# Kernel tuning notes

Measured on AMD Instinct MI355X. Metric: run time of the kernel, lower is better.

The kernel has to match this reference:

```python
import jax, jax.numpy as jnp
import numpy as np

N = 50000      # nodes
E = 500000     # edges
IN = 128       # in_channels
HID = 64       # hidden_channels
OUT = 128      # out_channels
H = 4          # heads
NEG_SLOPE = 0.2


def _glorot(key, shape):
    fan_in, fan_out = shape[0], shape[-1]
    lim = np.sqrt(6.0 / (fan_in + fan_out))
    return jax.random.uniform(key, shape, jnp.float32, -lim, lim)


def setup_inputs() -> dict:
    key = jax.random.key(0)
    ks = jax.random.split(key, 12)
    return {
        "x": jax.random.normal(ks[0], (N, IN), jnp.float32),
        "edge_index": jax.random.randint(ks[1], (2, E), 0, N, jnp.int64),
        "edge_weight": jax.random.uniform(ks[2], (E,), jnp.float32),
        # layer 1: IN -> H*HID
        "W1": _glorot(ks[3], (IN, H * HID)),
        "b1": jnp.zeros((H * HID,), jnp.float32),
        "att1": _glorot(ks[4], (H, HID)),
        # layer 2: HID -> H*HID  (update() means over heads -> HID features)
        "W2": _glorot(ks[5], (HID, H * HID)),
        "b2": jnp.zeros((H * HID,), jnp.float32),
        "att2": _glorot(ks[6], (H, HID)),
        # layer 3: HID -> H*OUT
        "W3": _glorot(ks[7], (HID, H * OUT)),
        "b3": jnp.zeros((H * OUT,), jnp.float32),
        "att3": _glorot(ks[8], (H, OUT)),
    }


def _gat_layer(x, W, b, att, src, dst, edge_weight, out_dim):
    # lin + reshape to [N, H, D]
    h = (x @ W + b).reshape(-1, H, out_dim)
    xj = h[src]                                   # gather source feats [E,H,D]
    alpha = jnp.sum(xj * att[None], axis=-1)      # per-edge att score [E,H]
    alpha = jax.nn.leaky_relu(alpha, NEG_SLOPE)
    alpha = alpha * edge_weight[:, None]
    alpha = jax.nn.softmax(alpha, axis=1)         # softmax over HEADS (dim=1, as in source)
    msg = xj * alpha[:, :, None]                  # [E,H,D]
    aggr = jax.ops.segment_sum(msg, dst, num_segments=N)  # scatter-add [N,H,D]
    return aggr.mean(axis=1)                      # update(): mean over heads -> [N,D]


def reference(x, edge_index, edge_weight, W1, b1, att1, W2, b2, att2, W3, b3, att3):
    src, dst = edge_index[0], edge_index[1]
    h = _gat_layer(x, W1, b1, att1, src, dst, edge_weight, HID)
    h = jax.nn.relu(h)
    h = _gat_layer(h, W2, b2, att2, src, dst, edge_weight, HID)
    h = jax.nn.relu(h)
    return _gat_layer(h, W3, b3, att3, src, dst, edge_weight, OUT)
```

## Files before the change

### kernel.cpp

```cpp
#include <hip/hip_runtime.h>
#include <hip/hip_bf16.h>

#define NHEAD 4
#define NEG 0.2f

typedef __bf16 bf16x8 __attribute__((ext_vector_type(8)));
typedef __bf16 bf16x4 __attribute__((ext_vector_type(4)));
typedef float f32x4 __attribute__((ext_vector_type(4)));

__device__ __forceinline__ float blo(unsigned u) { return __uint_as_float(u << 16); }
__device__ __forceinline__ float bhi(unsigned u) { return __uint_as_float(u & 0xffff0000u); }
__device__ __forceinline__ unsigned short fbits(float f) {
    __bf16 h = (__bf16)f;
    return *(unsigned short*)&h;
}


__global__ __launch_bounds__(256) void hist_k(const int* __restrict__ dst,
                                              int* __restrict__ deg, int E) {
    int e = blockIdx.x * 256 + threadIdx.x;
    if (e < E) atomicAdd(&deg[dst[e]], 1);
}

__global__ __launch_bounds__(256) void partial_k(const int* __restrict__ deg,
                                                 int* __restrict__ bsum, int n) {
    int t = threadIdx.x;
    int base = blockIdx.x * 2048 + t * 8;
    int s = 0;
#pragma unroll
    for (int i = 0; i < 8; ++i) {
        int idx = base + i;
        if (idx < n) s += deg[idx];
    }
#pragma unroll
    for (int off = 32; off; off >>= 1) s += __shfl_down(s, off, 64);
    __shared__ int ws[4];
    if ((t & 63) == 0) ws[t >> 6] = s;
    __syncthreads();
    if (t == 0) bsum[blockIdx.x] = ws[0] + ws[1] + ws[2] + ws[3];
}

__global__ __launch_bounds__(256) void bscan_k(const int* __restrict__ bsum,
                                               int* __restrict__ boff, int nb) {
    __shared__ int sh[256];
    int t = threadIdx.x;
    int v = (t < nb) ? bsum[t] : 0;
    sh[t] = v;
    __syncthreads();
    for (int off = 1; off < 256; off <<= 1) {
        int u = (t >= off) ? sh[t - off] : 0;
        __syncthreads();
        sh[t] += u;
        __syncthreads();
    }
    if (t < nb) boff[t] = sh[t] - v;
}

__global__ __launch_bounds__(256) void rescan_k(const int* __restrict__ deg,
                                                const int* __restrict__ boff,
                                                int* __restrict__ rowptr,
                                                int* __restrict__ fill,
                                                int n, int total) {
    __shared__ int ts[256];
    int t = threadIdx.x;
    int base = blockIdx.x * 2048 + t * 8;
    int v[8];
    int s = 0;
#pragma unroll
    for (int i = 0; i < 8; ++i) {
        int idx = base + i;
        v[i] = (idx < n) ? deg[idx] : 0;
        s += v[i];
    }
    ts[t] = s;
    __syncthreads();
    for (int off = 1; off < 256; off <<= 1) {
        int u = (t >= off) ? ts[t - off] : 0;
        __syncthreads();
        ts[t] += u;
        __syncthreads();
    }
    int run = boff[blockIdx.x] + ts[t] - s;
#pragma unroll
    for (int i = 0; i < 8; ++i) {
        int idx = base + i;
        if (idx < n) {
            rowptr[idx] = run;
            fill[idx] = run;
            run += v[i];
        }
    }
    if (blockIdx.x == 0 && t == 0) rowptr[n] = total;
}

__global__ __launch_bounds__(256) void scatter_k(const int* __restrict__ src,
                                                 const int* __restrict__ dst,
                                                 const float* __restrict__ ew,
                                                 int* __restrict__ fill,
                                                 int* __restrict__ srcs,
                                                 float* __restrict__ wsrt, int E) {
    int e = blockIdx.x * 256 + threadIdx.x;
    if (e < E) {
        int d = dst[e];
        int p = atomicAdd(&fill[d], 1);
        srcs[p] = src[e];
        wsrt[p] = ew[e];
    }
}


__global__ __launch_bounds__(256) void prep_k(const float* __restrict__ W1, const float* __restrict__ att1, const float* __restrict__ b1,
                                              const float* __restrict__ W2, const float* __restrict__ att2, const float* __restrict__ b2,
                                              const float* __restrict__ W3, const float* __restrict__ att3, const float* __restrict__ b3,
                                              float* __restrict__ v1, float* __restrict__ v2, float* __restrict__ v3,
                                              float* __restrict__ c1, float* __restrict__ c2, float* __restrict__ c3) {
    int tid = blockIdx.x * 256 + threadIdx.x;
    if (tid < 512) {
        int h = tid >> 7, k = tid & 127;
        float p = 0.f;
        for (int d = 0; d < 64; ++d) p += W1[k * 256 + h * 64 + d] * att1[h * 64 + d];
        v1[h * 128 + k] = p;
    } else if (tid < 768) {
        int t = tid - 512, h = t >> 6, k = t & 63;
        float p = 0.f;
        for (int d = 0; d < 64; ++d) p += W2[k * 256 + h * 64 + d] * att2[h * 64 + d];
        v2[h * 64 + k] = p;
    } else if (tid < 1024) {
        int t = tid - 768, h = t >> 6, k = t & 63;
        float p = 0.f;
        for (int d = 0; d < 128; ++d) p += W3[k * 512 + h * 128 + d] * att3[h * 128 + d];
        v3[h * 64 + k] = p;
    } else if (tid < 1028) {
        int h = tid - 1024;
        float p = 0.f;
        for (int d = 0; d < 64; ++d) p += b1[h * 64 + d] * att1[h * 64 + d];
        c1[h] = p;
    } else if (tid < 1032) {
        int h = tid - 1028;
        float p = 0.f;
        for (int d = 0; d < 64; ++d) p += b2[h * 64 + d] * att2[h * 64 + d];
        c2[h] = p;
    } else if (tid < 1036) {
        int h = tid - 1032;
        float p = 0.f;
        for (int d = 0; d < 128; ++d) p += b3[h * 128 + d] * att3[h * 128 + d];
        c3[h] = p;
    }
}


__global__ __launch_bounds__(256) void wpack3_k(const float* __restrict__ W1,
                                                const float* __restrict__ W2,
                                                const float* __restrict__ W3,
                                                unsigned short* __restrict__ Ws1,
                                                unsigned short* __restrict__ Ws2,
                                                unsigned short* __restrict__ Ws3) {
    int tid = blockIdx.x * 256 + threadIdx.x;
    if (tid < 32768) {
        int d = tid >> 9, r = tid & 511, h = r >> 7, k = r & 127;
        Ws1[tid] = fbits(W1[k * 256 + h * 64 + d]);
    } else if (tid < 49152) {
        int t = tid - 32768;
        int d = t >> 8, r = t & 255, h = r >> 6, k = r & 63;
        Ws2[t] = fbits(W2[k * 256 + h * 64 + d]);
    } else if (tid < 81920) {
        int t = tid - 49152;
        int d = t >> 8, r = t & 255, h = r >> 6, k = r & 63;
        Ws3[t] = fbits(W3[k * 512 + h * 128 + d]);
    }
}


__global__ __launch_bounds__(256) void xpack_score_k(const float* __restrict__ x,
                                                     const float* __restrict__ v1,
                                                     const float* __restrict__ c1,
                                                     unsigned* __restrict__ xb,
                                                     float* __restrict__ s, int n) {
    int gt = blockIdx.x * 256 + threadIdx.x;
    int node = gt >> 6, lane = gt & 63;
    if (node >= n) return;
    float2 xv = ((const float2*)(x + (size_t)node * 128))[lane];
    xb[(size_t)node * 64 + lane] = (unsigned)fbits(xv.x) | ((unsigned)fbits(xv.y) << 16);
    int d0 = 2 * lane;
    float p0 = xv.x * v1[0 * 128 + d0] + xv.y * v1[0 * 128 + d0 + 1];
    float p1 = xv.x * v1[1 * 128 + d0] + xv.y * v1[1 * 128 + d0 + 1];
    float p2 = xv.x * v1[2 * 128 + d0] + xv.y * v1[2 * 128 + d0 + 1];
    float p3 = xv.x * v1[3 * 128 + d0] + xv.y * v1[3 * 128 + d0 + 1];
#pragma unroll
    for (int off = 32; off; off >>= 1) {
        p0 += __shfl_xor(p0, off, 64);
        p1 += __shfl_xor(p1, off, 64);
        p2 += __shfl_xor(p2, off, 64);
        p3 += __shfl_xor(p3, off, 64);
    }
    if (lane == 0)
        *(float4*)&s[(size_t)node * 4] = make_float4(p0 + c1[0], p1 + c1[1], p2 + c1[2], p3 + c1[3]);
}


__global__ __launch_bounds__(256) void alpha_k(const int* __restrict__ srcs,
                                               const float* __restrict__ wsrt,
                                               const float* __restrict__ s,
                                               float* __restrict__ alpha, int E) {
    int e = blockIdx.x * 256 + threadIdx.x;
    if (e >= E) return;
    int sn = srcs[e];
    float w = wsrt[e];
    float4 sv = *(const float4*)&s[(size_t)sn * NHEAD];
    float a0 = (sv.x > 0.f ? sv.x : NEG * sv.x) * w;
    float a1 = (sv.y > 0.f ? sv.y : NEG * sv.y) * w;
    float a2 = (sv.z > 0.f ? sv.z : NEG * sv.z) * w;
    float a3 = (sv.w > 0.f ? sv.w : NEG * sv.w) * w;
    float m = fmaxf(fmaxf(a0, a1), fmaxf(a2, a3));
    float e0 = __expf(a0 - m), e1 = __expf(a1 - m);
    float e2 = __expf(a2 - m), e3 = __expf(a3 - m);
    float inv = 0.25f / (e0 + e1 + e2 + e3);
    *(float4*)&alpha[(size_t)e * 4] = make_float4(e0 * inv, e1 * inv, e2 * inv, e3 * inv);
}


template <int K, int D, bool LAST>
__global__ __launch_bounds__(256) void fused_k(const int* __restrict__ rowptr,
                                               const int* __restrict__ srcs,
                                               const float* __restrict__ alpha,
                                               const unsigned* __restrict__ xb,
                                               const unsigned short* __restrict__ Ws,
                                               const float* __restrict__ bias,
                                               const float* __restrict__ vnext,
                                               const float* __restrict__ cnext,
                                               unsigned short* __restrict__ aout,
                                               float* __restrict__ fout,
                                               float* __restrict__ snext,
                                               int n) {
    constexpr int HK = 4 * K;
    constexpr int KS = HK / 32;
    constexpr int NC = D / 16;
    constexpr int CW = NC / 4;
    constexpr int ROWB = HK + 8;
    constexpr int DW = K / 32;

    __shared__ __bf16 gh[16 * ROWB];
    __shared__ __bf16 gl[16 * ROWB];
    __shared__ float4 A_lds[16];
    __shared__ float4 sc_lds[4][16];

    int t = threadIdx.x;
    int r0 = blockIdx.x * 16;
    int n4 = t >> 4, sl = t & 15;
    int node = r0 + n4;

    float acc[4][2 * DW];
#pragma unroll
    for (int h = 0; h < 4; ++h)
#pragma unroll
        for (int j = 0; j < 2 * DW; ++j) acc[h][j] = 0.f;
    float4 aA = make_float4(0.f, 0.f, 0.f, 0.f);

    auto accum = [&](float4 al, const unsigned* u) {
#pragma unroll
        for (int j = 0; j < DW; ++j) {
            float x0 = blo(u[j]), x1 = bhi(u[j]);
            acc[0][2 * j] += al.x * x0; acc[0][2 * j + 1] += al.x * x1;
            acc[1][2 * j] += al.y * x0; acc[1][2 * j + 1] += al.y * x1;
            acc[2][2 * j] += al.z * x0; acc[2][2 * j + 1] += al.z * x1;
            acc[3][2 * j] += al.w * x0; acc[3][2 * j + 1] += al.w * x1;
        }
        aA.x += al.x; aA.y += al.y; aA.z += al.z; aA.w += al.w;
    };

    if (node < n) {
        int beg = rowptr[node], end = rowptr[node + 1];
        int e = beg;
        for (; e + 1 < end; e += 2) {
            int snA = srcs[e], snB = srcs[e + 1];
            float4 alA = *(const float4*)&alpha[(size_t)e * 4];
            float4 alB = *(const float4*)&alpha[(size_t)(e + 1) * 4];
            unsigned uA[DW], uB[DW];
            if constexpr (DW == 4) {
                uint4 ta = ((const uint4*)xb)[(size_t)snA * 16 + sl];
                uint4 tb = ((const uint4*)xb)[(size_t)snB * 16 + sl];
                uA[0] = ta.x; uA[1] = ta.y; uA[2] = ta.z; uA[3] = ta.w;
                uB[0] = tb.x; uB[1] = tb.y; uB[2] = tb.z; uB[3] = tb.w;
            } else {
                uint2 ta = ((const uint2*)xb)[(size_t)snA * 16 + sl];
                uint2 tb = ((const uint2*)xb)[(size_t)snB * 16 + sl];
                uA[0] = ta.x; uA[1] = ta.y;
                uB[0] = tb.x; uB[1] = tb.y;
            }
            accum(alA, uA);
            accum(alB, uB);
        }
        if (e < end) {
            int sn = srcs[e];
            float4 al = *(const float4*)&alpha[(size_t)e * 4];
            unsigned u[DW];
            if constexpr (DW == 4) {
                uint4 ta = ((const uint4*)xb)[(size_t)sn * 16 + sl];
                u[0] = ta.x; u[1] = ta.y; u[2] = ta.z; u[3] = ta.w;
            } else {
                uint2 ta = ((const uint2*)xb)[(size_t)sn * 16 + sl];
                u[0] = ta.x; u[1] = ta.y;
            }
            accum(al, u);
        }
    }

    {
        size_t gbase = (size_t)n4 * ROWB;
#pragma unroll
        for (int h = 0; h < 4; ++h) {
            if constexpr (DW == 4) {
                bf16x8 vh, vl;
#pragma unroll
                for (int j = 0; j < 8; ++j) {
                    __bf16 hi = (__bf16)acc[h][j];
                    vh[j] = hi;
                    vl[j] = (__bf16)(acc[h][j] - (float)hi);
                }
                *(bf16x8*)&gh[gbase + h * K + sl * 8] = vh;
                *(bf16x8*)&gl[gbase + h * K + sl * 8] = vl;
            } else {
                bf16x4 vh, vl;
#pragma unroll
                for (int j = 0; j < 4; ++j) {
                    __bf16 hi = (__bf16)acc[h][j];
                    vh[j] = hi;
                    vl[j] = (__bf16)(acc[h][j] - (float)hi);
                }
                *(bf16x4*)&gh[gbase + h * K + sl * 4] = vh;
                *(bf16x4*)&gl[gbase + h * K + sl * 4] = vl;
            }
        }
        if (sl == 0) A_lds[n4] = aA;
    }
    __syncthreads();

    int wid = t >> 6, lane = t & 63;
    int lrow = lane & 15, gq = lane >> 4;

    f32x4 acc2[CW];
#pragma unroll
    for (int cw = 0; cw < CW; ++cw)
#pragma unroll
        for (int r = 0; r < 4; ++r) acc2[cw][r] = 0.f;

    const __bf16* wsp = (const __bf16*)Ws;
#pragma unroll
    for (int ks = 0; ks < KS; ++ks) {
        bf16x8 fh = *(const bf16x8*)&gh[(size_t)lrow * ROWB + ks * 32 + gq * 8];
        bf16x8 fl = *(const bf16x8*)&gl[(size_t)lrow * ROWB + ks * 32 + gq * 8];
#pragma unroll
        for (int cw = 0; cw < CW; ++cw) {
            int c = wid * CW + cw;
            bf16x8 bfr = *(const bf16x8*)(wsp + (size_t)(c * 16 + lrow) * HK + ks * 32 + gq * 8);
            acc2[cw] = __builtin_amdgcn_mfma_f32_16x16x32_bf16(fh, bfr, acc2[cw], 0, 0, 0);
            acc2[cw] = __builtin_amdgcn_mfma_f32_16x16x32_bf16(fl, bfr, acc2[cw], 0, 0, 0);
        }
    }

    float4 Ar[4];
#pragma unroll
    for (int r = 0; r < 4; ++r) Ar[r] = A_lds[gq * 4 + r];

    float sc[4][4];
#pragma unroll
    for (int h = 0; h < 4; ++h)
#pragma unroll
        for (int r = 0; r < 4; ++r) sc[h][r] = 0.f;

#pragma unroll
    for (int cw = 0; cw < CW; ++cw) {
        int col = (wid * CW + cw) * 16 + lrow;
        float bb0 = bias[0 * D + col], bb1 = bias[1 * D + col];
        float bb2 = bias[2 * D + col], bb3 = bias[3 * D + col];
        float vv0 = 0.f, vv1 = 0.f, vv2 = 0.f, vv3 = 0.f;
        if constexpr (!LAST) {
            vv0 = vnext[0 * D + col]; vv1 = vnext[1 * D + col];
            vv2 = vnext[2 * D + col]; vv3 = vnext[3 * D + col];
        }
#pragma unroll
        for (int r = 0; r < 4; ++r) {
            float val = acc2[cw][r] + Ar[r].x * bb0 + Ar[r].y * bb1 + Ar[r].z * bb2 + Ar[r].w * bb3;
            int row = r0 + gq * 4 + r;
            if constexpr (LAST) {
                if (row < n) fout[(size_t)row * D + col] = val;
            } else {
                val = fmaxf(val, 0.f);
                if (row < n) aout[(size_t)row * D + col] = fbits(val);
                sc[0][r] += val * vv0;
                sc[1][r] += val * vv1;
                sc[2][r] += val * vv2;
                sc[3][r] += val * vv3;
            }
        }
    }

    if constexpr (!LAST) {
#pragma unroll
        for (int m = 1; m < 16; m <<= 1) {
#pragma unroll
            for (int h = 0; h < 4; ++h)
#pragma unroll
                for (int r = 0; r < 4; ++r) sc[h][r] += __shfl_xor(sc[h][r], m, 64);
        }
        if (lrow < 4) {
            int r = lrow;
            sc_lds[wid][gq * 4 + r] = make_float4(sc[0][r], sc[1][r], sc[2][r], sc[3][r]);
        }
        __syncthreads();
        if (t < 16) {
            int row = r0 + t;
            if (row < n) {
                float4 s0 = sc_lds[0][t], s1 = sc_lds[1][t];
                float4 s2 = sc_lds[2][t], s3 = sc_lds[3][t];
                *(float4*)&snext[(size_t)row * 4] =
                    make_float4(s0.x + s1.x + s2.x + s3.x + cnext[0],
                                s0.y + s1.y + s2.y + s3.y + cnext[1],
                                s0.z + s1.z + s2.z + s3.z + cnext[2],
                                s0.w + s1.w + s2.w + s3.w + cnext[3]);
            }
        }
    }
}


extern "C" void kernel_launch(void* const* d_in, const int* in_sizes, int n_in,
                              void* d_out, int out_size, void* d_ws, size_t ws_size,
                              hipStream_t stream) {
    const float* x    = (const float*)d_in[0];
    const int*   ei   = (const int*)d_in[1];
    const float* ew   = (const float*)d_in[2];
    const float* W1   = (const float*)d_in[3];
    const float* b1   = (const float*)d_in[4];
    const float* att1 = (const float*)d_in[5];
    const float* W2   = (const float*)d_in[6];
    const float* b2   = (const float*)d_in[7];
    const float* att2 = (const float*)d_in[8];
    const float* W3   = (const float*)d_in[9];
    const float* b3   = (const float*)d_in[10];
    const float* att3 = (const float*)d_in[11];

    const int N = in_sizes[0] / 128;
    const int E = in_sizes[2];
    const int* src = ei;
    const int* dst = ei + E;

    char* wp = (char*)d_ws;
    auto alloc = [&](size_t bytes) -> void* {
        void* p = (void*)wp;
        wp += (bytes + 511) & ~(size_t)511;
        return p;
    };
    int*   deg    = (int*)alloc((size_t)N * 4);
    int*   rowptr = (int*)alloc((size_t)(N + 1) * 4);
    int*   fill   = (int*)alloc((size_t)N * 4);
    int*   bsum   = (int*)alloc(256 * 4);
    int*   boff   = (int*)alloc(256 * 4);
    int*   srcs   = (int*)alloc((size_t)E * 4);
    float* wsrt   = (float*)alloc((size_t)E * 4);
    unsigned* xb  = (unsigned*)alloc((size_t)N * 64 * 4);
    float* s      = (float*)alloc((size_t)N * 4 * 4);
    float* alpha  = (float*)alloc((size_t)E * 4 * 4);
    unsigned short* a1 = (unsigned short*)alloc((size_t)N * 64 * 2);
    unsigned short* a2 = (unsigned short*)alloc((size_t)N * 64 * 2);
    float* v1 = (float*)alloc(512 * 4);
    float* v2 = (float*)alloc(256 * 4);
    float* v3 = (float*)alloc(256 * 4);
    float* c1 = (float*)alloc(16);
    float* c2 = (float*)alloc(16);
    float* c3 = (float*)alloc(16);
    unsigned short* Ws1 = (unsigned short*)alloc(32768 * 2);
    unsigned short* Ws2 = (unsigned short*)alloc(16384 * 2);
    unsigned short* Ws3 = (unsigned short*)alloc(32768 * 2);

    wpack3_k<<<320, 256, 0, stream>>>(W1, W2, W3, Ws1, Ws2, Ws3);
    prep_k<<<5, 256, 0, stream>>>(W1, att1, b1, W2, att2, b2, W3, att3, b3,
                                  v1, v2, v3, c1, c2, c3);
    int gx = (N * 64 + 255) / 256;
    xpack_score_k<<<gx, 256, 0, stream>>>(x, v1, c1, xb, s, N);

    hipMemsetAsync(deg, 0, (size_t)N * 4, stream);
    int ge = (E + 255) / 256;
    int nb = (N + 2047) / 2048;
    hist_k<<<ge, 256, 0, stream>>>(dst, deg, E);
    partial_k<<<nb, 256, 0, stream>>>(deg, bsum, N);
    bscan_k<<<1, 256, 0, stream>>>(bsum, boff, nb);
    rescan_k<<<nb, 256, 0, stream>>>(deg, boff, rowptr, fill, N, E);
    scatter_k<<<ge, 256, 0, stream>>>(src, dst, ew, fill, srcs, wsrt, E);

    int gf = (N + 15) / 16;

    alpha_k<<<ge, 256, 0, stream>>>(srcs, wsrt, s, alpha, E);
    fused_k<128, 64, false><<<gf, 256, 0, stream>>>(rowptr, srcs, alpha, xb, Ws1, b1,
                                                    v2, c2, a1, nullptr, s, N);

    alpha_k<<<ge, 256, 0, stream>>>(srcs, wsrt, s, alpha, E);
    fused_k<64, 64, false><<<gf, 256, 0, stream>>>(rowptr, srcs, alpha, (const unsigned*)a1,
                                                   Ws2, b2, v3, c3, a2, nullptr, s, N);

    alpha_k<<<ge, 256, 0, stream>>>(srcs, wsrt, s, alpha, E);
    fused_k<64, 128, true><<<gf, 256, 0, stream>>>(rowptr, srcs, alpha, (const unsigned*)a2,
                                                   Ws3, b3, nullptr, nullptr, nullptr,
                                                   (float*)d_out, nullptr, N);
}
```

Baseline: 253.8 us.

## Fuse per-edge alpha computation into aggregation kernel and swizzle LDS layout

Removes the separate alpha_k kernel and computes the per-edge softmax-over-heads inside the fused aggregation loop from the source node's score and the edge weight. A second score buffer is used to ping-pong, so no kernel reads and writes the same score array. The edge loop is unrolled to 4 edges, the LDS staging drops row padding in favour of an XOR swizzle to avoid bank conflicts, and launch bounds request 4 blocks per CU. This saves three kernel launches and the E*16-byte alpha write and read per layer, at the cost of recomputing exp per edge for each of the 16 threads handling a node.

```diff
diff --git a/kernel.cpp b/kernel.cpp
--- a/kernel.cpp
+++ b/kernel.cpp
@@ -198,15 +198,8 @@
 }
 
 
-__global__ __launch_bounds__(256) void alpha_k(const int* __restrict__ srcs,
-                                               const float* __restrict__ wsrt,
-                                               const float* __restrict__ s,
-                                               float* __restrict__ alpha, int E) {
-    int e = blockIdx.x * 256 + threadIdx.x;
-    if (e >= E) return;
-    int sn = srcs[e];
-    float w = wsrt[e];
-    float4 sv = *(const float4*)&s[(size_t)sn * NHEAD];
+__device__ __forceinline__ float4 edge_alpha(const float* __restrict__ s, int sn, float w) {
+    float4 sv = *(const float4*)&s[(size_t)sn * 4];
     float a0 = (sv.x > 0.f ? sv.x : NEG * sv.x) * w;
     float a1 = (sv.y > 0.f ? sv.y : NEG * sv.y) * w;
     float a2 = (sv.z > 0.f ? sv.z : NEG * sv.z) * w;
@@ -215,32 +208,32 @@
     float e0 = __expf(a0 - m), e1 = __expf(a1 - m);
     float e2 = __expf(a2 - m), e3 = __expf(a3 - m);
     float inv = 0.25f / (e0 + e1 + e2 + e3);
-    *(float4*)&alpha[(size_t)e * 4] = make_float4(e0 * inv, e1 * inv, e2 * inv, e3 * inv);
+    return make_float4(e0 * inv, e1 * inv, e2 * inv, e3 * inv);
 }
 
 
 template <int K, int D, bool LAST>
-__global__ __launch_bounds__(256) void fused_k(const int* __restrict__ rowptr,
-                                               const int* __restrict__ srcs,
-                                               const float* __restrict__ alpha,
-                                               const unsigned* __restrict__ xb,
-                                               const unsigned short* __restrict__ Ws,
-                                               const float* __restrict__ bias,
-                                               const float* __restrict__ vnext,
-                                               const float* __restrict__ cnext,
-                                               unsigned short* __restrict__ aout,
-                                               float* __restrict__ fout,
-                                               float* __restrict__ snext,
-                                               int n) {
+__global__ __launch_bounds__(256, 4) void fused_k(const int* __restrict__ rowptr,
+                                                  const int* __restrict__ srcs,
+                                                  const float* __restrict__ wsrt,
+                                                  const float* __restrict__ sprev,
+                                                  const unsigned* __restrict__ xb,
+                                                  const unsigned short* __restrict__ Ws,
+                                                  const float* __restrict__ bias,
+                                                  const float* __restrict__ vnext,
+                                                  const float* __restrict__ cnext,
+                                                  unsigned short* __restrict__ aout,
+                                                  float* __restrict__ fout,
+                                                  float* __restrict__ snext,
+                                                  int n) {
     constexpr int HK = 4 * K;
     constexpr int KS = HK / 32;
     constexpr int NC = D / 16;
     constexpr int CW = NC / 4;
-    constexpr int ROWB = HK + 8;
     constexpr int DW = K / 32;
 
-    __shared__ __bf16 gh[16 * ROWB];
-    __shared__ __bf16 gl[16 * ROWB];
+    __shared__ __bf16 gh[16 * HK];
+    __shared__ __bf16 gl[16 * HK];
     __shared__ float4 A_lds[16];
     __shared__ float4 sc_lds[4][16];
 
@@ -256,6 +249,15 @@
         for (int j = 0; j < 2 * DW; ++j) acc[h][j] = 0.f;
     float4 aA = make_float4(0.f, 0.f, 0.f, 0.f);
 
+    auto load_u = [&](int sn, unsigned* u) {
+        if constexpr (DW == 4) {
+            uint4 ta = ((const uint4*)xb)[(size_t)sn * 16 + sl];
+            u[0] = ta.x; u[1] = ta.y; u[2] = ta.z; u[3] = ta.w;
+        } else {
+            uint2 ta = ((const uint2*)xb)[(size_t)sn * 16 + sl];
+            u[0] = ta.x; u[1] = ta.y;
+        }
+    };
     auto accum = [&](float4 al, const unsigned* u) {
 #pragma unroll
         for (int j = 0; j < DW; ++j) {
@@ -271,42 +273,30 @@
     if (node < n) {
         int beg = rowptr[node], end = rowptr[node + 1];
         int e = beg;
-        for (; e + 1 < end; e += 2) {
-            int snA = srcs[e], snB = srcs[e + 1];
-            float4 alA = *(const float4*)&alpha[(size_t)e * 4];
-            float4 alB = *(const float4*)&alpha[(size_t)(e + 1) * 4];
-            unsigned uA[DW], uB[DW];
-            if constexpr (DW == 4) {
-                uint4 ta = ((const uint4*)xb)[(size_t)snA * 16 + sl];
-                uint4 tb = ((const uint4*)xb)[(size_t)snB * 16 + sl];
-                uA[0] = ta.x; uA[1] = ta.y; uA[2] = ta.z; uA[3] = ta.w;
-                uB[0] = tb.x; uB[1] = tb.y; uB[2] = tb.z; uB[3] = tb.w;
-            } else {
-                uint2 ta = ((const uint2*)xb)[(size_t)snA * 16 + sl];
-                uint2 tb = ((const uint2*)xb)[(size_t)snB * 16 + sl];
-                uA[0] = ta.x; uA[1] = ta.y;
-                uB[0] = tb.x; uB[1] = tb.y;
-            }
-            accum(alA, uA);
-            accum(alB, uB);
-        }
-        if (e < end) {
+        for (; e + 3 < end; e += 4) {
+            int sn0 = srcs[e], sn1 = srcs[e + 1], sn2 = srcs[e + 2], sn3 = srcs[e + 3];
+            float w0 = wsrt[e], w1 = wsrt[e + 1], w2 = wsrt[e + 2], w3 = wsrt[e + 3];
+            unsigned u0[DW], u1[DW], u2[DW], u3[DW];
+            load_u(sn0, u0); load_u(sn1, u1); load_u(sn2, u2); load_u(sn3, u3);
+            float4 al0 = edge_alpha(sprev, sn0, w0);
+            float4 al1 = edge_alpha(sprev, sn1, w1);
+            float4 al2 = edge_alpha(sprev, sn2, w2);
+            float4 al3 = edge_alpha(sprev, sn3, w3);
+            accum(al0, u0); accum(al1, u1); accum(al2, u2); accum(al3, u3);
+        }
+        for (; e < end; ++e) {
             int sn = srcs[e];
-            float4 al = *(const float4*)&alpha[(size_t)e * 4];
             unsigned u[DW];
-            if constexpr (DW == 4) {
-                uint4 ta = ((const uint4*)xb)[(size_t)sn * 16 + sl];
-                u[0] = ta.x; u[1] = ta.y; u[2] = ta.z; u[3] = ta.w;
-            } else {
-                uint2 ta = ((const uint2*)xb)[(size_t)sn * 16 + sl];
-                u[0] = ta.x; u[1] = ta.y;
-            }
+            load_u(sn, u);
+            float4 al = edge_alpha(sprev, sn, wsrt[e]);
             accum(al, u);
         }
     }
 
     {
-        size_t gbase = (size_t)n4 * ROWB;
+        char* ghb = (char*)gh + (size_t)n4 * (HK * 2);
+        char* glb = (char*)gl + (size_t)n4 * (HK * 2);
+        int sw = (n4 & 7) << 4;
 #pragma unroll
         for (int h = 0; h < 4; ++h) {
             if constexpr (DW == 4) {
@@ -317,8 +307,9 @@
                     vh[j] = hi;
                     vl[j] = (__bf16)(acc[h][j] - (float)hi);
                 }
-                *(bf16x8*)&gh[gbase + h * K + sl * 8] = vh;
-                *(bf16x8*)&gl[gbase + h * K + sl * 8] = vl;
+                int bo = (h * K + sl * 8) * 2;
+                *(bf16x8*)(ghb + (bo ^ sw)) = vh;
+                *(bf16x8*)(glb + (bo ^ sw)) = vl;
             } else {
                 bf16x4 vh, vl;
 #pragma unroll
@@ -327,8 +318,9 @@
                     vh[j] = hi;
                     vl[j] = (__bf16)(acc[h][j] - (float)hi);
                 }
-                *(bf16x4*)&gh[gbase + h * K + sl * 4] = vh;
-                *(bf16x4*)&gl[gbase + h * K + sl * 4] = vl;
+                int bo = (h * K + sl * 4) * 2;
+                *(bf16x4*)(ghb + (bo ^ sw)) = vh;
+                *(bf16x4*)(glb + (bo ^ sw)) = vl;
             }
         }
         if (sl == 0) A_lds[n4] = aA;
@@ -345,10 +337,14 @@
         for (int r = 0; r < 4; ++r) acc2[cw][r] = 0.f;
 
     const __bf16* wsp = (const __bf16*)Ws;
+    const char* ghr = (const char*)gh + (size_t)lrow * (HK * 2);
+    const char* glr = (const char*)gl + (size_t)lrow * (HK * 2);
+    int swr = (lrow & 7) << 4;
 #pragma unroll
     for (int ks = 0; ks < KS; ++ks) {
-        bf16x8 fh = *(const bf16x8*)&gh[(size_t)lrow * ROWB + ks * 32 + gq * 8];
-        bf16x8 fl = *(const bf16x8*)&gl[(size_t)lrow * ROWB + ks * 32 + gq * 8];
+        int bo = ks * 64 + gq * 16;
+        bf16x8 fh = *(const bf16x8*)(ghr + (bo ^ swr));
+        bf16x8 fl = *(const bf16x8*)(glr + (bo ^ swr));
 #pragma unroll
         for (int cw = 0; cw < CW; ++cw) {
             int c = wid * CW + cw;
@@ -460,7 +456,7 @@
     float* wsrt   = (float*)alloc((size_t)E * 4);
     unsigned* xb  = (unsigned*)alloc((size_t)N * 64 * 4);
     float* s      = (float*)alloc((size_t)N * 4 * 4);
-    float* alpha  = (float*)alloc((size_t)E * 4 * 4);
+    float* s2     = (float*)alloc((size_t)N * 4 * 4);
     unsigned short* a1 = (unsigned short*)alloc((size_t)N * 64 * 2);
     unsigned short* a2 = (unsigned short*)alloc((size_t)N * 64 * 2);
     float* v1 = (float*)alloc(512 * 4);
@@ -490,16 +486,13 @@
 
     int gf = (N + 15) / 16;
 
-    alpha_k<<<ge, 256, 0, stream>>>(srcs, wsrt, s, alpha, E);
-    fused_k<128, 64, false><<<gf, 256, 0, stream>>>(rowptr, srcs, alpha, xb, Ws1, b1,
-                                                    v2, c2, a1, nullptr, s, N);
-
-    alpha_k<<<ge, 256, 0, stream>>>(srcs, wsrt, s, alpha, E);
-    fused_k<64, 64, false><<<gf, 256, 0, stream>>>(rowptr, srcs, alpha, (const unsigned*)a1,
+    fused_k<128, 64, false><<<gf, 256, 0, stream>>>(rowptr, srcs, wsrt, s, xb, Ws1, b1,
+                                                    v2, c2, a1, nullptr, s2, N);
+
+    fused_k<64, 64, false><<<gf, 256, 0, stream>>>(rowptr, srcs, wsrt, s2, (const unsigned*)a1,
                                                    Ws2, b2, v3, c3, a2, nullptr, s, N);
 
-    alpha_k<<<ge, 256, 0, stream>>>(srcs, wsrt, s, alpha, E);
-    fused_k<64, 128, true><<<gf, 256, 0, stream>>>(rowptr, srcs, alpha, (const unsigned*)a2,
+    fused_k<64, 128, true><<<gf, 256, 0, stream>>>(rowptr, srcs, wsrt, s, (const unsigned*)a2,
                                                    Ws3, b3, nullptr, nullptr, nullptr,
                                                    (float*)d_out, nullptr, N);
 }
```

New measurement: 257.1 us. Within noise of the previous version (+1.3%).
